# Optimization experiments

Hardware: AMD Instinct MI355X
Metric: run time of the kernel (lower is better)

## Reference

```python
import jax, jax.numpy as jnp
import numpy as np

N_NODES = 50000
N_EDGES = 800000
IN_CH, HIDDEN, OUT_CH = 64, 16, 8


def setup_inputs() -> dict:
    key = jax.random.key(0)
    ks = jax.random.split(key, 8)
    x = jax.random.normal(ks[0], (N_NODES, IN_CH), dtype=jnp.float32)
    edge_index = jax.random.randint(ks[1], (2, N_EDGES), 0, N_NODES, dtype=jnp.int64)
    # SAGEConv params: lin_l (neighbor aggregate, has bias), lin_r (root, no bias)
    s1 = 1.0 / np.sqrt(IN_CH)
    s2 = 1.0 / np.sqrt(HIDDEN)
    W1l = jax.random.uniform(ks[2], (HIDDEN, IN_CH), jnp.float32, -s1, s1)
    W1r = jax.random.uniform(ks[3], (HIDDEN, IN_CH), jnp.float32, -s1, s1)
    b1 = jax.random.uniform(ks[4], (HIDDEN,), jnp.float32, -s1, s1)
    W2l = jax.random.uniform(ks[5], (OUT_CH, HIDDEN), jnp.float32, -s2, s2)
    W2r = jax.random.uniform(ks[6], (OUT_CH, HIDDEN), jnp.float32, -s2, s2)
    b2 = jax.random.uniform(ks[7], (OUT_CH,), jnp.float32, -s2, s2)
    return {"x": x, "W1l": W1l, "W1r": W1r, "b1": b1,
            "W2l": W2l, "W2r": W2r, "b2": b2, "edge_index": edge_index}


def _sage_conv(x, src, dst, Wl, Wr, b, n_nodes):
    # mean-aggregate neighbor features: gather from src, scatter-mean to dst
    msg_sum = jax.ops.segment_sum(x[src], dst, num_segments=n_nodes)  # [N, d]
    deg = jax.ops.segment_sum(jnp.ones((src.shape[0], 1), x.dtype), dst,
                              num_segments=n_nodes)                    # [N, 1]
    aggr = msg_sum / jnp.maximum(deg, 1.0)
    # out = lin_l(aggr) + lin_r(x); bias lives in lin_l
    return aggr @ Wl.T + x @ Wr.T + b


def reference(x, W1l, W1r, b1, W2l, W2r, b2, edge_index):
    src, dst = edge_index[0], edge_index[1]
    n = x.shape[0]
    h = jax.nn.relu(_sage_conv(x, src, dst, W1l, W1r, b1, n))
    # F.dropout(p=0.1, training=self.training): identity in eval mode
    return _sage_conv(h, src, dst, W2l, W2r, b2, n)
```

## Files before the change

### kernel.cpp

```cpp
#include <hip/hip_runtime.h>

#define IN_CH 64
#define HID   16
#define OUTC  8
#define BINSHIFT 6
#define BINCAP  (1 << BINSHIFT)
#define CHUNK   2048

typedef _Float16 half2_t __attribute__((ext_vector_type(2)));
typedef _Float16 half8_t __attribute__((ext_vector_type(8)));


__global__ __launch_bounds__(256) void build_xform(
    const float* __restrict__ x,
    const int*   __restrict__ esrc,
    const int*   __restrict__ edst,
    const float* __restrict__ W1l,
    const float* __restrict__ W1r,
    const float* __restrict__ b1,
    int* __restrict__ cur,
    unsigned short* __restrict__ adj,
    _Float16* __restrict__ y1h,
    float* __restrict__ r1,
    int n_nodes, int n_edges, int nb_scatter)
{
    __shared__ __align__(16) float sWl[HID * 68];
    __shared__ __align__(16) float sWr[HID * 68];
    __shared__ __align__(16) float sx[16 * 68];
    __shared__ float sb1[HID];

    int b   = blockIdx.x;
    int tid = threadIdx.x;

    if (b < nb_scatter) {
        int slice = b & 7;
        int chunk = b >> 3;
        int lo = (int)(((long long)slice       * n_nodes) >> 3);
        int hi = (int)(((long long)(slice + 1) * n_nodes) >> 3);
        int base = chunk * CHUNK;
#pragma unroll
        for (int j = 0; j < CHUNK / 256; ++j) {
            int e = base + j * 256 + tid;
            if (e < n_edges) {
                int d = edst[e];
                if (d >= lo && d < hi) {
                    int pos = atomicAdd(&cur[d], 1);
                    if (pos < BINCAP)
                        adj[((size_t)d << BINSHIFT) + pos] =
                            (unsigned short)esrc[e];
                }
            }
        }
        return;
    }

    for (int i = tid; i < HID * IN_CH; i += 256) {
        int c = i >> 6, k = i & 63;
        sWl[c * 68 + k] = W1l[i];
        sWr[c * 68 + k] = W1r[i];
    }
    if (tid < HID) sb1[tid] = b1[tid];

    int nl   = tid >> 4;
    int c    = tid & 15;
    int node = (b - nb_scatter) * 16 + nl;

    if (node < n_nodes)
        *(float4*)&sx[nl * 68 + c * 4] =
            *(const float4*)&x[(size_t)node * IN_CH + c * 4];
    __syncthreads();
    if (node >= n_nodes) return;

    float accL = 0.f, accR = 0.f;
#pragma unroll
    for (int k4 = 0; k4 < 16; ++k4) {
        float4 xv = *(const float4*)&sx [nl * 68 + k4 * 4];
        float4 wl = *(const float4*)&sWl[c  * 68 + k4 * 4];
        float4 wr = *(const float4*)&sWr[c  * 68 + k4 * 4];
        accL = fmaf(xv.x, wl.x, accL); accL = fmaf(xv.y, wl.y, accL);
        accL = fmaf(xv.z, wl.z, accL); accL = fmaf(xv.w, wl.w, accL);
        accR = fmaf(xv.x, wr.x, accR); accR = fmaf(xv.y, wr.y, accR);
        accR = fmaf(xv.z, wr.z, accR); accR = fmaf(xv.w, wr.w, accR);
    }
    y1h[(size_t)node * HID + c] = (_Float16)accL;
    r1 [(size_t)node * HID + c] = accR + sb1[c];
}

#define ACC8(v)                                                          \
    do {                                                                 \
        half2_t p01 = {(v).s0, (v).s1}, p23 = {(v).s2, (v).s3};          \
        half2_t p45 = {(v).s4, (v).s5}, p67 = {(v).s6, (v).s7};          \
        s0 = __builtin_amdgcn_fdot2(p01, k10, s0, false);                \
        s1 = __builtin_amdgcn_fdot2(p01, k01, s1, false);                \
        s2 = __builtin_amdgcn_fdot2(p23, k10, s2, false);                \
        s3 = __builtin_amdgcn_fdot2(p23, k01, s3, false);                \
        s4 = __builtin_amdgcn_fdot2(p45, k10, s4, false);                \
        s5 = __builtin_amdgcn_fdot2(p45, k01, s5, false);                \
        s6 = __builtin_amdgcn_fdot2(p67, k10, s6, false);                \
        s7 = __builtin_amdgcn_fdot2(p67, k01, s7, false);                \
    } while (0)

__global__ __launch_bounds__(256) void fused_gather(
    const float* __restrict__ r1,
    const _Float16* __restrict__ y1h,
    const int*   __restrict__ cur,
    const unsigned short* __restrict__ adj,
    const float* __restrict__ W2l, const float* __restrict__ W2r,
    const float* __restrict__ b2,
    _Float16* __restrict__ y2h, float* __restrict__ r2out,
    int n_nodes)
{
    __shared__ float sW2l[HID * OUTC];
    __shared__ float sW2r[HID * OUTC];
    __shared__ float sb2[OUTC];
    __shared__ float sh[32 * 17];

    int tid = threadIdx.x;
    for (int i = tid; i < HID * OUTC; i += 256) {
        int o = i >> 4, k = i & 15;
        sW2l[k * OUTC + o] = W2l[i];
        sW2r[k * OUTC + o] = W2r[i];
    }
    if (tid < OUTC) sb2[tid] = b2[tid];

    int nl   = tid >> 3;
    int t    = tid & 7;
    int h    = t >> 2;
    int ep   = t & 3;
    int node = blockIdx.x * 32 + nl;
    bool real = node < n_nodes;

    const half2_t k10 = {(_Float16)1.f, (_Float16)0.f};
    const half2_t k01 = {(_Float16)0.f, (_Float16)1.f};

    if (real) {
        int deg = cur[node];
        if (deg > BINCAP) deg = BINCAP;
        int iters = deg >> 2;
        float s0 = 0.f, s1 = 0.f, s2 = 0.f, s3 = 0.f;
        float s4 = 0.f, s5 = 0.f, s6 = 0.f, s7 = 0.f;
        const _Float16* yq = y1h + h * 8;
        const unsigned short* row = adj + ((size_t)node << BINSHIFT);
        const ushort4* ap = (const ushort4*)row;
        for (int it = ep; it < iters; it += 4) {
            ushort4 s = ap[it];
            half8_t v0 = *(const half8_t*)(yq + (size_t)s.x * HID);
            half8_t v1 = *(const half8_t*)(yq + (size_t)s.y * HID);
            half8_t v2 = *(const half8_t*)(yq + (size_t)s.z * HID);
            half8_t v3 = *(const half8_t*)(yq + (size_t)s.w * HID);
            ACC8(v0); ACC8(v1); ACC8(v2); ACC8(v3);
        }
        for (int g = (iters << 2) + ep; g < deg; g += 4) {
            half8_t v = *(const half8_t*)(yq + (size_t)row[g] * HID);
            ACC8(v);
        }
        s0 += __shfl_xor(s0, 1); s0 += __shfl_xor(s0, 2);
        s1 += __shfl_xor(s1, 1); s1 += __shfl_xor(s1, 2);
        s2 += __shfl_xor(s2, 1); s2 += __shfl_xor(s2, 2);
        s3 += __shfl_xor(s3, 1); s3 += __shfl_xor(s3, 2);
        s4 += __shfl_xor(s4, 1); s4 += __shfl_xor(s4, 2);
        s5 += __shfl_xor(s5, 1); s5 += __shfl_xor(s5, 2);
        s6 += __shfl_xor(s6, 1); s6 += __shfl_xor(s6, 2);
        s7 += __shfl_xor(s7, 1); s7 += __shfl_xor(s7, 2);

        if (ep == 0) {
            float inv = 1.0f / fmaxf((float)deg, 1.0f);
            const float* rr = &r1[(size_t)node * HID + h * 8];
            float4 ra = *(const float4*)(rr);
            float4 rb = *(const float4*)(rr + 4);
            float* shp = &sh[nl * 17 + h * 8];
            shp[0] = fmaxf(fmaf(s0, inv, ra.x), 0.f);
            shp[1] = fmaxf(fmaf(s1, inv, ra.y), 0.f);
            shp[2] = fmaxf(fmaf(s2, inv, ra.z), 0.f);
            shp[3] = fmaxf(fmaf(s3, inv, ra.w), 0.f);
            shp[4] = fmaxf(fmaf(s4, inv, rb.x), 0.f);
            shp[5] = fmaxf(fmaf(s5, inv, rb.y), 0.f);
            shp[6] = fmaxf(fmaf(s6, inv, rb.z), 0.f);
            shp[7] = fmaxf(fmaf(s7, inv, rb.w), 0.f);
        }
    }
    __syncthreads();
    if (!real) return;

    const float* hrow = &sh[nl * 17];
    float al = 0.f, ar = sb2[t];
#pragma unroll
    for (int k = 0; k < HID; ++k) {
        float hv = hrow[k];
        al = fmaf(hv, sW2l[k * OUTC + t], al);
        ar = fmaf(hv, sW2r[k * OUTC + t], ar);
    }
    y2h[(size_t)node * OUTC + t] = (_Float16)al;
    r2out[(size_t)node * OUTC + t] = ar;
}

__global__ __launch_bounds__(256) void gather_out(
    const _Float16* __restrict__ y2h,
    const int*   __restrict__ cur,
    const unsigned short* __restrict__ adj,
    float* __restrict__ out,
    int n_nodes)
{
    int tid  = threadIdx.x;
    int node = blockIdx.x * 64 + (tid >> 2);
    if (node >= n_nodes) return;
    int ep = tid & 3;

    int deg = cur[node];
    if (deg > BINCAP) deg = BINCAP;
    int iters = deg >> 2;
    const unsigned short* row = adj + ((size_t)node << BINSHIFT);
    const ushort4* ap = (const ushort4*)row;

    const half2_t k10 = {(_Float16)1.f, (_Float16)0.f};
    const half2_t k01 = {(_Float16)0.f, (_Float16)1.f};

    float s0 = 0.f, s1 = 0.f, s2 = 0.f, s3 = 0.f;
    float s4 = 0.f, s5 = 0.f, s6 = 0.f, s7 = 0.f;
    for (int it = ep; it < iters; it += 4) {
        ushort4 s = ap[it];
        half8_t v0 = *(const half8_t*)(y2h + (size_t)s.x * OUTC);
        half8_t v1 = *(const half8_t*)(y2h + (size_t)s.y * OUTC);
        half8_t v2 = *(const half8_t*)(y2h + (size_t)s.z * OUTC);
        half8_t v3 = *(const half8_t*)(y2h + (size_t)s.w * OUTC);
        ACC8(v0); ACC8(v1); ACC8(v2); ACC8(v3);
    }
    for (int g = (iters << 2) + ep; g < deg; g += 4) {
        half8_t v = *(const half8_t*)(y2h + (size_t)row[g] * OUTC);
        ACC8(v);
    }
    s0 += __shfl_xor(s0, 1); s0 += __shfl_xor(s0, 2);
    s1 += __shfl_xor(s1, 1); s1 += __shfl_xor(s1, 2);
    s2 += __shfl_xor(s2, 1); s2 += __shfl_xor(s2, 2);
    s3 += __shfl_xor(s3, 1); s3 += __shfl_xor(s3, 2);
    s4 += __shfl_xor(s4, 1); s4 += __shfl_xor(s4, 2);
    s5 += __shfl_xor(s5, 1); s5 += __shfl_xor(s5, 2);
    s6 += __shfl_xor(s6, 1); s6 += __shfl_xor(s6, 2);
    s7 += __shfl_xor(s7, 1); s7 += __shfl_xor(s7, 2);
    if (ep != 0) return;

    float inv = 1.0f / fmaxf((float)deg, 1.0f);
    float* op = out + (size_t)node * OUTC;
    float4 c0 = *(float4*)op;
    float4 c1 = *(float4*)(op + 4);
    c0.x = fmaf(s0, inv, c0.x); c0.y = fmaf(s1, inv, c0.y);
    c0.z = fmaf(s2, inv, c0.z); c0.w = fmaf(s3, inv, c0.w);
    c1.x = fmaf(s4, inv, c1.x); c1.y = fmaf(s5, inv, c1.y);
    c1.z = fmaf(s6, inv, c1.z); c1.w = fmaf(s7, inv, c1.w);
    *(float4*)op = c0;
    *(float4*)(op + 4) = c1;
}

extern "C" void kernel_launch(void* const* d_in, const int* in_sizes, int n_in,
                              void* d_out, int out_size, void* d_ws, size_t ws_size,
                              hipStream_t stream)
{
    const float* x   = (const float*)d_in[0];
    const float* W1l = (const float*)d_in[1];
    const float* W1r = (const float*)d_in[2];
    const float* b1  = (const float*)d_in[3];
    const float* W2l = (const float*)d_in[4];
    const float* W2r = (const float*)d_in[5];
    const float* b2  = (const float*)d_in[6];
    const int*   ei  = (const int*)d_in[7];

    int n_nodes = in_sizes[0] / IN_CH;
    int n_edges = in_sizes[7] / 2;
    const int* esrc = ei;
    const int* edst = ei + n_edges;

    float* out = (float*)d_out;

    char* wsb = (char*)d_ws;
    _Float16* y1h = (_Float16*)wsb;
    _Float16* y2h = y1h + (size_t)n_nodes * HID;
    float* r1 = (float*)(y2h + (size_t)n_nodes * OUTC);
    int* cur  = (int*)(r1 + (size_t)n_nodes * HID);
    unsigned short* adj = (unsigned short*)(cur + n_nodes);

    dim3 blk(256);
    int n_chunks   = (n_edges + CHUNK - 1) / CHUNK;
    int nb_scatter = n_chunks * 8;
    int nb_node    = (n_nodes + 15) / 16;

    hipMemsetAsync(cur, 0, (size_t)n_nodes * sizeof(int), stream);

    build_xform<<<dim3(nb_scatter + nb_node), blk, 0, stream>>>(
        x, esrc, edst, W1l, W1r, b1, cur, adj, y1h, r1,
        n_nodes, n_edges, nb_scatter);

    fused_gather<<<dim3((n_nodes + 31) / 32), blk, 0, stream>>>(
        r1, y1h, cur, adj, W2l, W2r, b2, y2h, out, n_nodes);

    gather_out<<<dim3((n_nodes + 63) / 64), blk, 0, stream>>>(
        y2h, cur, adj, out, n_nodes);
}
```

Before: 132.2 us.

## Merge all stages into one persistent cooperative kernel with grid syncs

Replaces the memset and three separate kernel launches with a single cooperative persistent kernel of 1024 blocks. The stages (zeroing degree counters, edge binning plus layer-1 transform, layer-1 gather with layer-2 transform, final gather) loop over tiles and are separated by grid-wide barriers. This removes launch gaps and the memset call. In exchange it adds grid barrier cost, requires all 1024 blocks to be co-resident, and serialises stages that previously overlapped within a launch.

```diff
diff --git a/kernel.cpp b/kernel.cpp
--- a/kernel.cpp
+++ b/kernel.cpp
@@ -1,4 +1,7 @@
 #include <hip/hip_runtime.h>
+#include <hip/hip_cooperative_groups.h>
+
+namespace cg = cooperative_groups;
 
 #define IN_CH 64
 #define HID   16
@@ -6,35 +9,79 @@
 #define BINSHIFT 6
 #define BINCAP  (1 << BINSHIFT)
 #define CHUNK   2048
+#define NBLK    1024
 
 typedef _Float16 half2_t __attribute__((ext_vector_type(2)));
 typedef _Float16 half8_t __attribute__((ext_vector_type(8)));
 
 
-__global__ __launch_bounds__(256) void build_xform(
+#define ACC8(v)                                                          \
+    do {                                                                 \
+        half2_t p01 = {(v).s0, (v).s1}, p23 = {(v).s2, (v).s3};          \
+        half2_t p45 = {(v).s4, (v).s5}, p67 = {(v).s6, (v).s7};          \
+        s0 = __builtin_amdgcn_fdot2(p01, k10, s0, false);                \
+        s1 = __builtin_amdgcn_fdot2(p01, k01, s1, false);                \
+        s2 = __builtin_amdgcn_fdot2(p23, k10, s2, false);                \
+        s3 = __builtin_amdgcn_fdot2(p23, k01, s3, false);                \
+        s4 = __builtin_amdgcn_fdot2(p45, k10, s4, false);                \
+        s5 = __builtin_amdgcn_fdot2(p45, k01, s5, false);                \
+        s6 = __builtin_amdgcn_fdot2(p67, k10, s6, false);                \
+        s7 = __builtin_amdgcn_fdot2(p67, k01, s7, false);                \
+    } while (0)
+
+__global__ __launch_bounds__(256) void persistent_all(
     const float* __restrict__ x,
     const int*   __restrict__ esrc,
     const int*   __restrict__ edst,
     const float* __restrict__ W1l,
     const float* __restrict__ W1r,
     const float* __restrict__ b1,
+    const float* __restrict__ W2l,
+    const float* __restrict__ W2r,
+    const float* __restrict__ b2,
     int* __restrict__ cur,
     unsigned short* __restrict__ adj,
     _Float16* __restrict__ y1h,
+    _Float16* __restrict__ y2h,
     float* __restrict__ r1,
-    int n_nodes, int n_edges, int nb_scatter)
+    float* __restrict__ out,
+    int n_nodes, int n_edges,
+    int n_sc_tiles, int n_x_tiles, int n_g2_tiles, int n_g3_tiles)
 {
+    cg::grid_group grid = cg::this_grid();
+
     __shared__ __align__(16) float sWl[HID * 68];
     __shared__ __align__(16) float sWr[HID * 68];
     __shared__ __align__(16) float sx[16 * 68];
+    __shared__ float sW2l[HID * OUTC];
+    __shared__ float sW2r[HID * OUTC];
     __shared__ float sb1[HID];
-
-    int b   = blockIdx.x;
+    __shared__ float sb2[OUTC];
+    __shared__ float sh[32 * 17];
+
+    int nb  = gridDim.x;
+    int b0  = blockIdx.x;
     int tid = threadIdx.x;
 
-    if (b < nb_scatter) {
-        int slice = b & 7;
-        int chunk = b >> 3;
+    for (int i = tid; i < HID * IN_CH; i += 256) {
+        int c = i >> 6, k = i & 63;
+        sWl[c * 68 + k] = W1l[i];
+        sWr[c * 68 + k] = W1r[i];
+    }
+    for (int i = tid; i < HID * OUTC; i += 256) {
+        int o = i >> 4, k = i & 15;
+        sW2l[k * OUTC + o] = W2l[i];
+        sW2r[k * OUTC + o] = W2r[i];
+    }
+    if (tid < HID)  sb1[tid] = b1[tid];
+    if (tid < OUTC) sb2[tid] = b2[tid];
+
+    for (int i = b0 * 256 + tid; i < n_nodes; i += nb * 256) cur[i] = 0;
+    grid.sync();
+
+    for (int t = b0; t < n_sc_tiles; t += nb) {
+        int slice = t & 7;
+        int chunk = t >> 3;
         int lo = (int)(((long long)slice       * n_nodes) >> 3);
         int hi = (int)(((long long)(slice + 1) * n_nodes) >> 3);
         int base = chunk * CHUNK;
@@ -51,204 +98,161 @@
                 }
             }
         }
-        return;
-    }
-
-    for (int i = tid; i < HID * IN_CH; i += 256) {
-        int c = i >> 6, k = i & 63;
-        sWl[c * 68 + k] = W1l[i];
-        sWr[c * 68 + k] = W1r[i];
-    }
-    if (tid < HID) sb1[tid] = b1[tid];
-
-    int nl   = tid >> 4;
-    int c    = tid & 15;
-    int node = (b - nb_scatter) * 16 + nl;
-
-    if (node < n_nodes)
-        *(float4*)&sx[nl * 68 + c * 4] =
-            *(const float4*)&x[(size_t)node * IN_CH + c * 4];
-    __syncthreads();
-    if (node >= n_nodes) return;
-
-    float accL = 0.f, accR = 0.f;
+    }
+
+    {
+        int nl = tid >> 4;
+        int c  = tid & 15;
+        for (int t = b0; t < n_x_tiles; t += nb) {
+            int node = t * 16 + nl;
+            __syncthreads();
+            if (node < n_nodes)
+                *(float4*)&sx[nl * 68 + c * 4] =
+                    *(const float4*)&x[(size_t)node * IN_CH + c * 4];
+            __syncthreads();
+            if (node >= n_nodes) continue;
+
+            float accL = 0.f, accR = 0.f;
 #pragma unroll
-    for (int k4 = 0; k4 < 16; ++k4) {
-        float4 xv = *(const float4*)&sx [nl * 68 + k4 * 4];
-        float4 wl = *(const float4*)&sWl[c  * 68 + k4 * 4];
-        float4 wr = *(const float4*)&sWr[c  * 68 + k4 * 4];
-        accL = fmaf(xv.x, wl.x, accL); accL = fmaf(xv.y, wl.y, accL);
-        accL = fmaf(xv.z, wl.z, accL); accL = fmaf(xv.w, wl.w, accL);
-        accR = fmaf(xv.x, wr.x, accR); accR = fmaf(xv.y, wr.y, accR);
-        accR = fmaf(xv.z, wr.z, accR); accR = fmaf(xv.w, wr.w, accR);
-    }
-    y1h[(size_t)node * HID + c] = (_Float16)accL;
-    r1 [(size_t)node * HID + c] = accR + sb1[c];
-}
-
-#define ACC8(v)                                                          \
-    do {                                                                 \
-        half2_t p01 = {(v).s0, (v).s1}, p23 = {(v).s2, (v).s3};          \
-        half2_t p45 = {(v).s4, (v).s5}, p67 = {(v).s6, (v).s7};          \
-        s0 = __builtin_amdgcn_fdot2(p01, k10, s0, false);                \
-        s1 = __builtin_amdgcn_fdot2(p01, k01, s1, false);                \
-        s2 = __builtin_amdgcn_fdot2(p23, k10, s2, false);                \
-        s3 = __builtin_amdgcn_fdot2(p23, k01, s3, false);                \
-        s4 = __builtin_amdgcn_fdot2(p45, k10, s4, false);                \
-        s5 = __builtin_amdgcn_fdot2(p45, k01, s5, false);                \
-        s6 = __builtin_amdgcn_fdot2(p67, k10, s6, false);                \
-        s7 = __builtin_amdgcn_fdot2(p67, k01, s7, false);                \
-    } while (0)
-
-__global__ __launch_bounds__(256) void fused_gather(
-    const float* __restrict__ r1,
-    const _Float16* __restrict__ y1h,
-    const int*   __restrict__ cur,
-    const unsigned short* __restrict__ adj,
-    const float* __restrict__ W2l, const float* __restrict__ W2r,
-    const float* __restrict__ b2,
-    _Float16* __restrict__ y2h, float* __restrict__ r2out,
-    int n_nodes)
-{
-    __shared__ float sW2l[HID * OUTC];
-    __shared__ float sW2r[HID * OUTC];
-    __shared__ float sb2[OUTC];
-    __shared__ float sh[32 * 17];
-
-    int tid = threadIdx.x;
-    for (int i = tid; i < HID * OUTC; i += 256) {
-        int o = i >> 4, k = i & 15;
-        sW2l[k * OUTC + o] = W2l[i];
-        sW2r[k * OUTC + o] = W2r[i];
-    }
-    if (tid < OUTC) sb2[tid] = b2[tid];
-
-    int nl   = tid >> 3;
-    int t    = tid & 7;
-    int h    = t >> 2;
-    int ep   = t & 3;
-    int node = blockIdx.x * 32 + nl;
-    bool real = node < n_nodes;
-
-    const half2_t k10 = {(_Float16)1.f, (_Float16)0.f};
-    const half2_t k01 = {(_Float16)0.f, (_Float16)1.f};
-
-    if (real) {
-        int deg = cur[node];
-        if (deg > BINCAP) deg = BINCAP;
-        int iters = deg >> 2;
-        float s0 = 0.f, s1 = 0.f, s2 = 0.f, s3 = 0.f;
-        float s4 = 0.f, s5 = 0.f, s6 = 0.f, s7 = 0.f;
-        const _Float16* yq = y1h + h * 8;
-        const unsigned short* row = adj + ((size_t)node << BINSHIFT);
-        const ushort4* ap = (const ushort4*)row;
-        for (int it = ep; it < iters; it += 4) {
-            ushort4 s = ap[it];
-            half8_t v0 = *(const half8_t*)(yq + (size_t)s.x * HID);
-            half8_t v1 = *(const half8_t*)(yq + (size_t)s.y * HID);
-            half8_t v2 = *(const half8_t*)(yq + (size_t)s.z * HID);
-            half8_t v3 = *(const half8_t*)(yq + (size_t)s.w * HID);
-            ACC8(v0); ACC8(v1); ACC8(v2); ACC8(v3);
+            for (int k4 = 0; k4 < 16; ++k4) {
+                float4 xv = *(const float4*)&sx [nl * 68 + k4 * 4];
+                float4 wl = *(const float4*)&sWl[c  * 68 + k4 * 4];
+                float4 wr = *(const float4*)&sWr[c  * 68 + k4 * 4];
+                accL = fmaf(xv.x, wl.x, accL); accL = fmaf(xv.y, wl.y, accL);
+                accL = fmaf(xv.z, wl.z, accL); accL = fmaf(xv.w, wl.w, accL);
+                accR = fmaf(xv.x, wr.x, accR); accR = fmaf(xv.y, wr.y, accR);
+                accR = fmaf(xv.z, wr.z, accR); accR = fmaf(xv.w, wr.w, accR);
+            }
+            y1h[(size_t)node * HID + c] = (_Float16)accL;
+            r1 [(size_t)node * HID + c] = accR + sb1[c];
         }
-        for (int g = (iters << 2) + ep; g < deg; g += 4) {
-            half8_t v = *(const half8_t*)(yq + (size_t)row[g] * HID);
-            ACC8(v);
+    }
+    grid.sync();
+
+    {
+        int nl = tid >> 3;
+        int t8 = tid & 7;
+        int h  = t8 >> 2;
+        int ep = t8 & 3;
+        const half2_t k10 = {(_Float16)1.f, (_Float16)0.f};
+        const half2_t k01 = {(_Float16)0.f, (_Float16)1.f};
+
+        for (int t = b0; t < n_g2_tiles; t += nb) {
+            int node = t * 32 + nl;
+            bool real = node < n_nodes;
+            float s0 = 0.f, s1 = 0.f, s2 = 0.f, s3 = 0.f;
+            float s4 = 0.f, s5 = 0.f, s6 = 0.f, s7 = 0.f;
+            int deg = 0;
+            if (real) {
+                deg = cur[node];
+                if (deg > BINCAP) deg = BINCAP;
+                int iters = deg >> 2;
+                const _Float16* yq = y1h + h * 8;
+                const unsigned short* row = adj + ((size_t)node << BINSHIFT);
+                const ushort4* ap = (const ushort4*)row;
+                for (int it = ep; it < iters; it += 4) {
+                    ushort4 s = ap[it];
+                    half8_t v0 = *(const half8_t*)(yq + (size_t)s.x * HID);
+                    half8_t v1 = *(const half8_t*)(yq + (size_t)s.y * HID);
+                    half8_t v2 = *(const half8_t*)(yq + (size_t)s.z * HID);
+                    half8_t v3 = *(const half8_t*)(yq + (size_t)s.w * HID);
+                    ACC8(v0); ACC8(v1); ACC8(v2); ACC8(v3);
+                }
+                for (int g = (iters << 2) + ep; g < deg; g += 4) {
+                    half8_t v = *(const half8_t*)(yq + (size_t)row[g] * HID);
+                    ACC8(v);
+                }
+                s0 += __shfl_xor(s0, 1); s0 += __shfl_xor(s0, 2);
+                s1 += __shfl_xor(s1, 1); s1 += __shfl_xor(s1, 2);
+                s2 += __shfl_xor(s2, 1); s2 += __shfl_xor(s2, 2);
+                s3 += __shfl_xor(s3, 1); s3 += __shfl_xor(s3, 2);
+                s4 += __shfl_xor(s4, 1); s4 += __shfl_xor(s4, 2);
+                s5 += __shfl_xor(s5, 1); s5 += __shfl_xor(s5, 2);
+                s6 += __shfl_xor(s6, 1); s6 += __shfl_xor(s6, 2);
+                s7 += __shfl_xor(s7, 1); s7 += __shfl_xor(s7, 2);
+            }
+            __syncthreads();
+            if (real && ep == 0) {
+                float inv = 1.0f / fmaxf((float)deg, 1.0f);
+                const float* rr = &r1[(size_t)node * HID + h * 8];
+                float4 ra = *(const float4*)(rr);
+                float4 rb = *(const float4*)(rr + 4);
+                float* shp = &sh[nl * 17 + h * 8];
+                shp[0] = fmaxf(fmaf(s0, inv, ra.x), 0.f);
+                shp[1] = fmaxf(fmaf(s1, inv, ra.y), 0.f);
+                shp[2] = fmaxf(fmaf(s2, inv, ra.z), 0.f);
+                shp[3] = fmaxf(fmaf(s3, inv, ra.w), 0.f);
+                shp[4] = fmaxf(fmaf(s4, inv, rb.x), 0.f);
+                shp[5] = fmaxf(fmaf(s5, inv, rb.y), 0.f);
+                shp[6] = fmaxf(fmaf(s6, inv, rb.z), 0.f);
+                shp[7] = fmaxf(fmaf(s7, inv, rb.w), 0.f);
+            }
+            __syncthreads();
+            if (!real) continue;
+            const float* hrow = &sh[nl * 17];
+            float al = 0.f, ar = sb2[t8];
+#pragma unroll
+            for (int k = 0; k < HID; ++k) {
+                float hv = hrow[k];
+                al = fmaf(hv, sW2l[k * OUTC + t8], al);
+                ar = fmaf(hv, sW2r[k * OUTC + t8], ar);
+            }
+            y2h[(size_t)node * OUTC + t8] = (_Float16)al;
+            out[(size_t)node * OUTC + t8] = ar;
         }
-        s0 += __shfl_xor(s0, 1); s0 += __shfl_xor(s0, 2);
-        s1 += __shfl_xor(s1, 1); s1 += __shfl_xor(s1, 2);
-        s2 += __shfl_xor(s2, 1); s2 += __shfl_xor(s2, 2);
-        s3 += __shfl_xor(s3, 1); s3 += __shfl_xor(s3, 2);
-        s4 += __shfl_xor(s4, 1); s4 += __shfl_xor(s4, 2);
-        s5 += __shfl_xor(s5, 1); s5 += __shfl_xor(s5, 2);
-        s6 += __shfl_xor(s6, 1); s6 += __shfl_xor(s6, 2);
-        s7 += __shfl_xor(s7, 1); s7 += __shfl_xor(s7, 2);
-
-        if (ep == 0) {
+    }
+    grid.sync();
+
+    {
+        int nl = tid >> 2;
+        int ep = tid & 3;
+        const half2_t k10 = {(_Float16)1.f, (_Float16)0.f};
+        const half2_t k01 = {(_Float16)0.f, (_Float16)1.f};
+
+        for (int t = b0; t < n_g3_tiles; t += nb) {
+            int node = t * 64 + nl;
+            if (node >= n_nodes) continue;
+            int deg = cur[node];
+            if (deg > BINCAP) deg = BINCAP;
+            int iters = deg >> 2;
+            const unsigned short* row = adj + ((size_t)node << BINSHIFT);
+            const ushort4* ap = (const ushort4*)row;
+            float s0 = 0.f, s1 = 0.f, s2 = 0.f, s3 = 0.f;
+            float s4 = 0.f, s5 = 0.f, s6 = 0.f, s7 = 0.f;
+            for (int it = ep; it < iters; it += 4) {
+                ushort4 s = ap[it];
+                half8_t v0 = *(const half8_t*)(y2h + (size_t)s.x * OUTC);
+                half8_t v1 = *(const half8_t*)(y2h + (size_t)s.y * OUTC);
+                half8_t v2 = *(const half8_t*)(y2h + (size_t)s.z * OUTC);
+                half8_t v3 = *(const half8_t*)(y2h + (size_t)s.w * OUTC);
+                ACC8(v0); ACC8(v1); ACC8(v2); ACC8(v3);
+            }
+            for (int g = (iters << 2) + ep; g < deg; g += 4) {
+                half8_t v = *(const half8_t*)(y2h + (size_t)row[g] * OUTC);
+                ACC8(v);
+            }
+            s0 += __shfl_xor(s0, 1); s0 += __shfl_xor(s0, 2);
+            s1 += __shfl_xor(s1, 1); s1 += __shfl_xor(s1, 2);
+            s2 += __shfl_xor(s2, 1); s2 += __shfl_xor(s2, 2);
+            s3 += __shfl_xor(s3, 1); s3 += __shfl_xor(s3, 2);
+            s4 += __shfl_xor(s4, 1); s4 += __shfl_xor(s4, 2);
+            s5 += __shfl_xor(s5, 1); s5 += __shfl_xor(s5, 2);
+            s6 += __shfl_xor(s6, 1); s6 += __shfl_xor(s6, 2);
+            s7 += __shfl_xor(s7, 1); s7 += __shfl_xor(s7, 2);
+            if (ep != 0) continue;
+
             float inv = 1.0f / fmaxf((float)deg, 1.0f);
-            const float* rr = &r1[(size_t)node * HID + h * 8];
-            float4 ra = *(const float4*)(rr);
-            float4 rb = *(const float4*)(rr + 4);
-            float* shp = &sh[nl * 17 + h * 8];
-            shp[0] = fmaxf(fmaf(s0, inv, ra.x), 0.f);
-            shp[1] = fmaxf(fmaf(s1, inv, ra.y), 0.f);
-            shp[2] = fmaxf(fmaf(s2, inv, ra.z), 0.f);
-            shp[3] = fmaxf(fmaf(s3, inv, ra.w), 0.f);
-            shp[4] = fmaxf(fmaf(s4, inv, rb.x), 0.f);
-            shp[5] = fmaxf(fmaf(s5, inv, rb.y), 0.f);
-            shp[6] = fmaxf(fmaf(s6, inv, rb.z), 0.f);
-            shp[7] = fmaxf(fmaf(s7, inv, rb.w), 0.f);
+            float* op = out + (size_t)node * OUTC;
+            float4 c0 = *(float4*)op;
+            float4 c1 = *(float4*)(op + 4);
+            c0.x = fmaf(s0, inv, c0.x); c0.y = fmaf(s1, inv, c0.y);
+            c0.z = fmaf(s2, inv, c0.z); c0.w = fmaf(s3, inv, c0.w);
+            c1.x = fmaf(s4, inv, c1.x); c1.y = fmaf(s5, inv, c1.y);
+            c1.z = fmaf(s6, inv, c1.z); c1.w = fmaf(s7, inv, c1.w);
+            *(float4*)op = c0;
+            *(float4*)(op + 4) = c1;
         }
     }
-    __syncthreads();
-    if (!real) return;
-
-    const float* hrow = &sh[nl * 17];
-    float al = 0.f, ar = sb2[t];
-#pragma unroll
-    for (int k = 0; k < HID; ++k) {
-        float hv = hrow[k];
-        al = fmaf(hv, sW2l[k * OUTC + t], al);
-        ar = fmaf(hv, sW2r[k * OUTC + t], ar);
-    }
-    y2h[(size_t)node * OUTC + t] = (_Float16)al;
-    r2out[(size_t)node * OUTC + t] = ar;
-}
-
-__global__ __launch_bounds__(256) void gather_out(
-    const _Float16* __restrict__ y2h,
-    const int*   __restrict__ cur,
-    const unsigned short* __restrict__ adj,
-    float* __restrict__ out,
-    int n_nodes)
-{
-    int tid  = threadIdx.x;
-    int node = blockIdx.x * 64 + (tid >> 2);
-    if (node >= n_nodes) return;
-    int ep = tid & 3;
-
-    int deg = cur[node];
-    if (deg > BINCAP) deg = BINCAP;
-    int iters = deg >> 2;
-    const unsigned short* row = adj + ((size_t)node << BINSHIFT);
-    const ushort4* ap = (const ushort4*)row;
-
-    const half2_t k10 = {(_Float16)1.f, (_Float16)0.f};
-    const half2_t k01 = {(_Float16)0.f, (_Float16)1.f};
-
-    float s0 = 0.f, s1 = 0.f, s2 = 0.f, s3 = 0.f;
-    float s4 = 0.f, s5 = 0.f, s6 = 0.f, s7 = 0.f;
-    for (int it = ep; it < iters; it += 4) {
-        ushort4 s = ap[it];
-        half8_t v0 = *(const half8_t*)(y2h + (size_t)s.x * OUTC);
-        half8_t v1 = *(const half8_t*)(y2h + (size_t)s.y * OUTC);
-        half8_t v2 = *(const half8_t*)(y2h + (size_t)s.z * OUTC);
-        half8_t v3 = *(const half8_t*)(y2h + (size_t)s.w * OUTC);
-        ACC8(v0); ACC8(v1); ACC8(v2); ACC8(v3);
-    }
-    for (int g = (iters << 2) + ep; g < deg; g += 4) {
-        half8_t v = *(const half8_t*)(y2h + (size_t)row[g] * OUTC);
-        ACC8(v);
-    }
-    s0 += __shfl_xor(s0, 1); s0 += __shfl_xor(s0, 2);
-    s1 += __shfl_xor(s1, 1); s1 += __shfl_xor(s1, 2);
-    s2 += __shfl_xor(s2, 1); s2 += __shfl_xor(s2, 2);
-    s3 += __shfl_xor(s3, 1); s3 += __shfl_xor(s3, 2);
-    s4 += __shfl_xor(s4, 1); s4 += __shfl_xor(s4, 2);
-    s5 += __shfl_xor(s5, 1); s5 += __shfl_xor(s5, 2);
-    s6 += __shfl_xor(s6, 1); s6 += __shfl_xor(s6, 2);
-    s7 += __shfl_xor(s7, 1); s7 += __shfl_xor(s7, 2);
-    if (ep != 0) return;
-
-    float inv = 1.0f / fmaxf((float)deg, 1.0f);
-    float* op = out + (size_t)node * OUTC;
-    float4 c0 = *(float4*)op;
-    float4 c1 = *(float4*)(op + 4);
-    c0.x = fmaf(s0, inv, c0.x); c0.y = fmaf(s1, inv, c0.y);
-    c0.z = fmaf(s2, inv, c0.z); c0.w = fmaf(s3, inv, c0.w);
-    c1.x = fmaf(s4, inv, c1.x); c1.y = fmaf(s5, inv, c1.y);
-    c1.z = fmaf(s6, inv, c1.z); c1.w = fmaf(s7, inv, c1.w);
-    *(float4*)op = c0;
-    *(float4*)(op + 4) = c1;
 }
 
 extern "C" void kernel_launch(void* const* d_in, const int* in_sizes, int n_in,
@@ -278,20 +282,25 @@
     int* cur  = (int*)(r1 + (size_t)n_nodes * HID);
     unsigned short* adj = (unsigned short*)(cur + n_nodes);
 
-    dim3 blk(256);
     int n_chunks   = (n_edges + CHUNK - 1) / CHUNK;
-    int nb_scatter = n_chunks * 8;
-    int nb_node    = (n_nodes + 15) / 16;
-
-    hipMemsetAsync(cur, 0, (size_t)n_nodes * sizeof(int), stream);
-
-    build_xform<<<dim3(nb_scatter + nb_node), blk, 0, stream>>>(
-        x, esrc, edst, W1l, W1r, b1, cur, adj, y1h, r1,
-        n_nodes, n_edges, nb_scatter);
-
-    fused_gather<<<dim3((n_nodes + 31) / 32), blk, 0, stream>>>(
-        r1, y1h, cur, adj, W2l, W2r, b2, y2h, out, n_nodes);
-
-    gather_out<<<dim3((n_nodes + 63) / 64), blk, 0, stream>>>(
-        y2h, cur, adj, out, n_nodes);
+    int n_sc_tiles = n_chunks * 8;
+    int n_x_tiles  = (n_nodes + 15) / 16;
+    int n_g2_tiles = (n_nodes + 31) / 32;
+    int n_g3_tiles = (n_nodes + 63) / 64;
+
+    void* kx   = (void*)x;   void* ks   = (void*)esrc; void* kd  = (void*)edst;
+    void* kw1l = (void*)W1l; void* kw1r = (void*)W1r;  void* kb1 = (void*)b1;
+    void* kw2l = (void*)W2l; void* kw2r = (void*)W2r;  void* kb2 = (void*)b2;
+    void* kcur = (void*)cur; void* kadj = (void*)adj;
+    void* ky1  = (void*)y1h; void* ky2  = (void*)y2h;  void* kr1 = (void*)r1;
+    void* kout = (void*)out;
+
+    void* args[] = {
+        &kx, &ks, &kd, &kw1l, &kw1r, &kb1, &kw2l, &kw2r, &kb2,
+        &kcur, &kadj, &ky1, &ky2, &kr1, &kout,
+        &n_nodes, &n_edges, &n_sc_tiles, &n_x_tiles, &n_g2_tiles, &n_g3_tiles
+    };
+
+    hipLaunchCooperativeKernel((const void*)persistent_all,
+                               dim3(NBLK), dim3(256), args, 0, stream);
 }
```

Result: slower. 423.0 us (+219.8%).
